# Optimization experiments

Hardware: AMD Instinct MI355X
Metric: run time of the kernel (lower is better)

The kernel has to match this reference:

```python
import jax, jax.numpy as jnp
import numpy as np

H, I, C, B, T = 128, 270, 3, 1024, 270


def setup_inputs() -> dict:
    key = jax.random.key(0)
    ks = jax.random.split(key, 6)
    inp = {
        "x": jax.random.normal(ks[0], (B, T, I), dtype=jnp.float32),
        "Wf": jax.random.normal(ks[1], (H, I + H), dtype=jnp.float32) * 0.01,
        "Wi": jax.random.normal(ks[2], (H, I + H), dtype=jnp.float32) * 0.01,
        "Wc": jax.random.normal(ks[3], (H, I + H), dtype=jnp.float32) * 0.01,
        "Wo": jax.random.normal(ks[4], (H, I + H), dtype=jnp.float32) * 0.01,
        "Wy": jax.random.normal(ks[5], (C, H), dtype=jnp.float32) * 0.01,
        "bf": jnp.zeros((H,), jnp.float32),
        "bi": jnp.zeros((H,), jnp.float32),
        "bc": jnp.zeros((H,), jnp.float32),
        "bo": jnp.zeros((H,), jnp.float32),
        "by": jnp.zeros((C,), jnp.float32),
    }
    return inp


def _lstm_forward(x, Wf, Wi, Wc, Wo, Wy, bf, bi, bc, bo, by):
    # combined = [h_prev, x_t], so W[:, :H] acts on h, W[:, H:] acts on x.
    Wh = jnp.stack([Wf[:, :H], Wi[:, :H], Wc[:, :H], Wo[:, :H]])      # [4,H,H]
    Wx = jnp.stack([Wf[:, H:], Wi[:, H:], Wc[:, H:], Wo[:, H:]])      # [4,H,I]
    b = jnp.stack([bf, bi, bc, bo])                                   # [4,H]
    # Precompute input projections for all timesteps: one big GEMM.
    xp = jnp.einsum('bti,ghi->tbgh', x, Wx)                           # [T,B,4,H]

    def step(carry, xpt):
        h, c = carry
        pre = xpt + jnp.einsum('bh,gkh->bgk', h, Wh) + b              # [B,4,H]
        f = jax.nn.sigmoid(pre[:, 0])
        i = jax.nn.sigmoid(pre[:, 1])
        g = jnp.tanh(pre[:, 2])
        o = jax.nn.sigmoid(pre[:, 3])
        c_new = f * c + i * g
        h_new = o * jnp.tanh(c_new)
        return (h_new, c_new), h_new

    h0 = jnp.zeros((x.shape[0], H), x.dtype)
    c0 = jnp.zeros((x.shape[0], H), x.dtype)
    _, hs = jax.lax.scan(step, (h0, c0), xp)                          # hs: [T,B,H]
    all_hiddens = jnp.transpose(hs, (1, 0, 2))                        # [B,T,H]
    logits = jnp.einsum('bth,ch->btc', all_hiddens, Wy) + by
    all_outputs = jax.nn.softmax(logits, axis=-1)                     # [B,T,C]
    return all_hiddens, all_outputs


def reference(x, Wf, Wi, Wc, Wo, Wy, bf, bi, bc, bo, by):
    return _lstm_forward(x, Wf, Wi, Wc, Wo, Wy, bf, bi, bc, bo, by)
```

## Files before the change

### kernel.cpp

```cpp
#include <hip/hip_runtime.h>
#include <stdint.h>


typedef __attribute__((ext_vector_type(8))) short short8;
typedef __attribute__((ext_vector_type(4))) float f32x4;
typedef __attribute__((ext_vector_type(2))) float f32x2;
typedef __attribute__((ext_vector_type(4))) unsigned int uint4v;
typedef __attribute__((ext_vector_type(2))) unsigned int u32x2;
typedef unsigned short ush;

__device__ __forceinline__ ush f2bf(float f) {
    unsigned u = __float_as_uint(f);
    return (ush)((u + 0x7FFFu + ((u >> 16) & 1u)) >> 16);
}
__device__ __forceinline__ float bf2f(ush s) { return __uint_as_float(((unsigned)s) << 16); }
__device__ __forceinline__ void lds_barrier() {
    asm volatile("s_waitcnt lgkmcnt(0)" ::: "memory");
    __builtin_amdgcn_s_barrier();
    __builtin_amdgcn_sched_barrier(0);
    asm volatile("" ::: "memory");
}

__global__ __launch_bounds__(256) void pack_w(
    const float* __restrict__ Wf, const float* __restrict__ Wi,
    const float* __restrict__ Wc, const float* __restrict__ Wo,
    const float* __restrict__ bf_, const float* __restrict__ bi_,
    const float* __restrict__ bc_, const float* __restrict__ bo_,
    ush* __restrict__ Wxp, ush* __restrict__ Whp, float* __restrict__ bpk)
{
    int idx = blockIdx.x * 256 + threadIdx.x;
    if (idx < 512 * 288) {
        int u = idx / 288, i = idx - u * 288;
        int g = u >> 7, j = u & 127;
        const float* Wg = (g == 0) ? Wf : (g == 1) ? Wi : (g == 2) ? Wc : Wo;
        float v = (i < 270) ? Wg[(size_t)j * 398 + 128 + i] : 0.f;
        Wxp[idx] = f2bf(v);
    }
    if (idx < 512 * 128) {
        int u = idx >> 7, k = idx & 127;
        int g = u >> 7, j = u & 127;
        const float* Wg = (g == 0) ? Wf : (g == 1) ? Wi : (g == 2) ? Wc : Wo;
        Whp[idx] = f2bf(Wg[(size_t)j * 398 + k]);
    }
    if (idx < 512) {
        int g = idx >> 7, j = idx & 127;
        const float* bg = (g == 0) ? bf_ : (g == 1) ? bi_ : (g == 2) ? bc_ : bo_;
        bpk[idx] = bg[j];
    }
}

__global__ __launch_bounds__(256, 2) void xp_gemm(
    const float* __restrict__ x, const ush* __restrict__ Wxp,
    const float* __restrict__ bpk, ush* __restrict__ xpc, int t0)
{
    __shared__ ush A_lds[64 * 296];
    const int tid = threadIdx.x;
    const int l = tid & 63, w = tid >> 6;
    const int l16 = l & 15, lq = l >> 4;
    const size_t row0 = (size_t)blockIdx.x * 64;

    const int srow = tid >> 2, sgrp = tid & 3;
    const int r = (int)row0 + srow;
    const int b = r & 1023, tt = (r >> 10) + t0;
    const float* xrow = x + ((size_t)b * 270 + tt) * 270;
    f32x2 stg[9][4];
    #pragma unroll
    for (int ks = 0; ks < 9; ++ks) {
        const int col = ks * 32 + sgrp * 8;
        const float* p = xrow + col;
        if (col + 8 <= 270) {
            stg[ks][0] = *(const f32x2*)p;       stg[ks][1] = *(const f32x2*)(p + 2);
            stg[ks][2] = *(const f32x2*)(p + 4); stg[ks][3] = *(const f32x2*)(p + 6);
        } else {
            float tv[8];
            #pragma unroll
            for (int j = 0; j < 8; ++j) tv[j] = (col + j < 270) ? p[j] : 0.f;
            stg[ks][0] = (f32x2){tv[0], tv[1]}; stg[ks][1] = (f32x2){tv[2], tv[3]};
            stg[ks][2] = (f32x2){tv[4], tv[5]}; stg[ks][3] = (f32x2){tv[6], tv[7]};
        }
    }

    const ush* bptr = Wxp + ((size_t)(w * 128 + l16)) * 288 + lq * 8;
    short8 bA[8], bB[8];
    #pragma unroll
    for (int nt = 0; nt < 8; ++nt) bA[nt] = *(const short8*)(bptr + nt * 4608);
    float bias_v[8];
    #pragma unroll
    for (int nt = 0; nt < 8; ++nt) bias_v[nt] = bpk[w * 128 + nt * 16 + l16];

    {
        ush* wrow = &A_lds[srow * 296 + sgrp * 8];
        #pragma unroll
        for (int ks = 0; ks < 9; ++ks) {
            uint4v o;
            #pragma unroll
            for (int p2 = 0; p2 < 4; ++p2) {
                unsigned v;
                asm("v_cvt_pk_bf16_f32 %0, %1, %2"
                    : "=v"(v) : "v"(stg[ks][p2].x), "v"(stg[ks][p2].y));
                o[p2] = v;
            }
            *(uint4v*)(wrow + ks * 32) = o;
        }
    }
    lds_barrier();

    f32x4 acc[4][8];
    #pragma unroll
    for (int mt = 0; mt < 4; ++mt)
        #pragma unroll
        for (int nt = 0; nt < 8; ++nt)
            acc[mt][nt] = (f32x4){bias_v[nt], bias_v[nt], bias_v[nt], bias_v[nt]};

    #pragma unroll
    for (int ks = 0; ks < 9; ++ks) {
        short8* cur = (ks & 1) ? bB : bA;
        short8* nxt = (ks & 1) ? bA : bB;
        if (ks + 1 < 9) {
            const ush* np = bptr + (ks + 1) * 32;
            #pragma unroll
            for (int nt = 0; nt < 8; ++nt) nxt[nt] = *(const short8*)(np + nt * 4608);
        }
        short8 afr[4];
        #pragma unroll
        for (int mt = 0; mt < 4; ++mt)
            afr[mt] = *(const short8*)(&A_lds[(mt * 16 + l16) * 296 + ks * 32 + lq * 8]);
        #pragma unroll
        for (int mt = 0; mt < 4; ++mt)
            #pragma unroll
            for (int nt = 0; nt < 8; ++nt)
                acc[mt][nt] = __builtin_amdgcn_mfma_f32_16x16x32_bf16(
                    afr[mt], cur[nt], acc[mt][nt], 0, 0, 0);
    }

    const int tloc = (int)(row0 >> 10);
    const int bg0 = ((int)row0 & 1023) >> 4;
    #pragma unroll
    for (int mt = 0; mt < 4; ++mt)
        #pragma unroll
        for (int nt = 0; nt < 8; ++nt) {
            int u = w * 128 + nt * 16 + l16;
            ush* dst = xpc + ((size_t)(tloc * 64 + bg0 + mt) * 512 + u) * 16 + lq * 4;
            #pragma unroll
            for (int q = 0; q < 4; ++q) dst[q] = f2bf(acc[mt][nt][q]);
        }
}

#define STEPB(T, PS)                                                            \
  {                                                                             \
    const int t_ = (T);                                                         \
    const bool lw_ = (((w >> 2) ^ (t_ & 1)) == 0) && (t_ > t0);                 \
    short8 afr[4];                                                              \
    _Pragma("unroll") for (int kf = 0; kf < 4; ++kf) {                          \
      int off_ = ((l16 * 128 + kf * 32 + lq * 8) * 2) ^ ((l16 & 7) << 4);       \
      afr[kf] = *(const short8*)(hbase + cur * 4096 + off_);                    \
    }                                                                           \
    float xg_[4][4];                                                            \
    _Pragma("unroll") for (int g = 0; g < 4; ++g) {                             \
      u32x2 pv_ = PS[g];                                                        \
      xg_[g][0] = __uint_as_float(pv_.x << 16);                                 \
      xg_[g][1] = __uint_as_float(pv_.x & 0xffff0000u);                         \
      xg_[g][2] = __uint_as_float(pv_.y << 16);                                 \
      xg_[g][3] = __uint_as_float(pv_.y & 0xffff0000u);                         \
    }                                                                           \
    if (t_ + 2 < t1) {                                                          \
      const ush* pn_ = xb + (size_t)(t_ + 2 - t0) * TSTEP;                      \
      _Pragma("unroll") for (int g = 0; g < 4; ++g)                             \
        PS[g] = *(const u32x2*)(pn_ + go[g]);                                   \
    }                                                                           \
    f32x4 a0_[4], a1_[4];                                                       \
    _Pragma("unroll") for (int g = 0; g < 4; ++g) {                             \
      a0_[g] = (f32x4){xg_[g][0], xg_[g][1], xg_[g][2], xg_[g][3]};             \
      a1_[g] = (f32x4){0.f, 0.f, 0.f, 0.f};                                     \
    }                                                                           \
    _Pragma("unroll") for (int g = 0; g < 4; ++g) {                             \
      a0_[g] = __builtin_amdgcn_mfma_f32_16x16x32_bf16(afr[0], whf[g][0], a0_[g], 0, 0, 0); \
      a1_[g] = __builtin_amdgcn_mfma_f32_16x16x32_bf16(afr[2], whf[g][2], a1_[g], 0, 0, 0); \
      a0_[g] = __builtin_amdgcn_mfma_f32_16x16x32_bf16(afr[1], whf[g][1], a0_[g], 0, 0, 0); \
      a1_[g] = __builtin_amdgcn_mfma_f32_16x16x32_bf16(afr[3], whf[g][3], a1_[g], 0, 0, 0); \
    }                                                                           \
    f32x4 ay0_ = (f32x4){0.f, 0.f, 0.f, 0.f};                                   \
    f32x4 ay1_ = (f32x4){0.f, 0.f, 0.f, 0.f};                                   \
    if (lw_) {                            \
      ay0_ = __builtin_amdgcn_mfma_f32_16x16x32_bf16(afr[0], wyf[0], ay0_, 0, 0, 0); \
      ay1_ = __builtin_amdgcn_mfma_f32_16x16x32_bf16(afr[2], wyf[2], ay1_, 0, 0, 0); \
      ay0_ = __builtin_amdgcn_mfma_f32_16x16x32_bf16(afr[1], wyf[1], ay0_, 0, 0, 0); \
      ay1_ = __builtin_amdgcn_mfma_f32_16x16x32_bf16(afr[3], wyf[3], ay1_, 0, 0, 0); \
    }                                                                           \
    float hv_[4];                                                               \
    _Pragma("unroll") for (int q = 0; q < 4; ++q) {                             \
      float pf_ = fminf(fmaxf(a0_[0][q] + a1_[0][q], -20.f), 20.f);             \
      float pi_ = fminf(fmaxf(a0_[1][q] + a1_[1][q], -20.f), 20.f);             \
      float pc_ = fminf(fmaxf(a0_[2][q] + a1_[2][q], -10.f), 10.f);             \
      float po_ = fminf(fmaxf(a0_[3][q] + a1_[3][q], -20.f), 20.f);             \
      float df_ = 1.f + __expf(-pf_);                                           \
      float di_ = 1.f + __expf(-pi_);                                           \
      float ec2_ = __expf(-2.f * pc_);                                          \
      float dc_ = 1.f + ec2_;                                                   \
      float do2_ = 1.f + __expf(-po_);                                          \
      float didc_ = di_ * dc_;                                                  \
      float num_ = c[q] * didc_ + (1.f - ec2_) * df_;                           \
      float cn_ = num_ * __builtin_amdgcn_rcpf(df_ * didc_);                    \
      c[q] = cn_;                                                               \
      float cnc_ = fminf(fmaxf(cn_, -10.f), 10.f);                              \
      float et2_ = __expf(-2.f * cnc_);                                         \
      hv_[q] = (1.f - et2_) * __builtin_amdgcn_rcpf(do2_ * (1.f + et2_));       \
    }                                                                           \
    _Pragma("unroll") for (int q = 0; q < 4; ++q) {                             \
      int rr_ = lq * 4 + q;                                                     \
      int off_ = ((rr_ * 128 + jcol) * 2) ^ ((rr_ & 7) << 4);                   \
      *(ush*)(hbase + (cur ^ 1) * 4096 + off_) = f2bf(hv_[q]);                  \
      out0[(size_t)(b0 + rr_) * (270 * 128) + (size_t)t_ * 128 + jcol] = hv_[q];\
    }                                                                           \
    lds_barrier();                                                              \
       \
    if (lw_) {                                                                  \
      f32x4 ay_ = ay0_ + ay1_;                                                  \
      int ww_ = w & 3;                                                          \
      float L_ = ((ww_ == 0) ? ay_[0] : (ww_ == 1) ? ay_[1] : (ww_ == 2) ? ay_[2] : ay_[3]) + byl; \
      if (l16 >= 3) L_ = -1e30f;                                                \
      float m_ = fmaxf(L_, __shfl_xor(L_, 1));                                  \
      m_ = fmaxf(m_, __shfl_xor(m_, 2));                                        \
      float e_ = (l16 < 3) ? __expf(L_ - m_) : 0.f;                             \
      float s_ = e_ + __shfl_xor(e_, 1);                                        \
      s_ = s_ + __shfl_xor(s_, 2);                                              \
      if (l16 < 3)                                                              \
        out1[((size_t)(b0 + lq * 4 + ww_) * 270 + (t_ - 1)) * 3 + l16] = e_ * __builtin_amdgcn_rcpf(s_); \
    }                                                                           \
    cur ^= 1;                                                                   \
  }

__global__ __launch_bounds__(512) void lstm_scan(
    const ush* __restrict__ xpc, const ush* __restrict__ Whp,
    float* __restrict__ c_state, float* __restrict__ out0, float* __restrict__ out1,
    const float* __restrict__ Wy, const float* __restrict__ by, int t0, int t1)
{
    __shared__ ush h_lds[2][16 * 128];
    const int tid = threadIdx.x;
    const int l = tid & 63, w = tid >> 6;
    const int l16 = l & 15, lq = l >> 4;
    const int b0 = blockIdx.x * 16;
    const int jcol = w * 16 + l16;
    char* hbase = (char*)&h_lds[0][0];

    short8 whf[4][4];
    #pragma unroll
    for (int g = 0; g < 4; ++g) {
        const ush* bw = Whp + ((size_t)(g * 128 + jcol)) * 128 + lq * 8;
        #pragma unroll
        for (int kf = 0; kf < 4; ++kf) whf[g][kf] = *(const short8*)(bw + kf * 32);
    }
    short8 wyf[4];
    #pragma unroll
    for (int kf = 0; kf < 4; ++kf) {
        short8 fr;
        #pragma unroll
        for (int j = 0; j < 8; ++j)
            fr[j] = (l16 < 3) ? (short)f2bf(Wy[l16 * 128 + kf * 32 + lq * 8 + j]) : (short)0;
        wyf[kf] = fr;
    }
    const float byl = (l16 < 3) ? by[l16] : 0.f;

    {
        ush* hp = &h_lds[0][0];
        for (int idx = tid; idx < 2 * 16 * 128; idx += 512) hp[idx] = 0;
    }
    __syncthreads();

    int cur = 0;
    float c[4] = {0.f, 0.f, 0.f, 0.f};
    if (t0 != 0) {
        #pragma unroll
        for (int q = 0; q < 4; ++q)
            c[q] = c_state[(size_t)(b0 + lq * 4 + q) * 128 + jcol];
        for (int idx = tid; idx < 2048; idx += 512) {
            int rr = idx >> 7, k = idx & 127;
            float hvv = out0[(size_t)(b0 + rr) * (270 * 128) + (size_t)(t0 - 1) * 128 + k];
            int off = ((rr * 128 + k) * 2) ^ ((rr & 7) << 4);
            *(ush*)(hbase + off) = f2bf(hvv);
        }
        __syncthreads();
    }

    const size_t TSTEP = (size_t)64 * 512 * 16;
    const ush* xb = xpc + (size_t)blockIdx.x * 8192;
    int go[4];
    #pragma unroll
    for (int g = 0; g < 4; ++g) go[g] = (g * 128 + jcol) * 16 + lq * 4;

    u32x2 Pa[4], Pb[4];
    #pragma unroll
    for (int g = 0; g < 4; ++g) Pa[g] = *(const u32x2*)(xb + go[g]);
    #pragma unroll
    for (int g = 0; g < 4; ++g) Pb[g] = *(const u32x2*)(xb + TSTEP + go[g]);

    for (int t = t0; t < t1; t += 2) {
        STEPB(t, Pa)
        STEPB(t + 1, Pb)
    }

    {
        short8 afr[4];
        #pragma unroll
        for (int kf = 0; kf < 4; ++kf) {
            int off = ((l16 * 128 + kf * 32 + lq * 8) * 2) ^ ((l16 & 7) << 4);
            afr[kf] = *(const short8*)(hbase + cur * 4096 + off);
        }
        if (w < 4) {
            f32x4 ay = (f32x4){0.f, 0.f, 0.f, 0.f};
            ay = __builtin_amdgcn_mfma_f32_16x16x32_bf16(afr[0], wyf[0], ay, 0, 0, 0);
            ay = __builtin_amdgcn_mfma_f32_16x16x32_bf16(afr[1], wyf[1], ay, 0, 0, 0);
            ay = __builtin_amdgcn_mfma_f32_16x16x32_bf16(afr[2], wyf[2], ay, 0, 0, 0);
            ay = __builtin_amdgcn_mfma_f32_16x16x32_bf16(afr[3], wyf[3], ay, 0, 0, 0);
            float L = ((w == 0) ? ay[0] : (w == 1) ? ay[1] : (w == 2) ? ay[2] : ay[3]) + byl;
            if (l16 >= 3) L = -1e30f;
            float m = fmaxf(L, __shfl_xor(L, 1));
            m = fmaxf(m, __shfl_xor(m, 2));
            float e = (l16 < 3) ? __expf(L - m) : 0.f;
            float s = e + __shfl_xor(e, 1);
            s = s + __shfl_xor(s, 2);
            if (l16 < 3)
                out1[((size_t)(b0 + lq * 4 + w) * 270 + (t1 - 1)) * 3 + l16] =
                    e * __builtin_amdgcn_rcpf(s);
        }
    }

    if (t1 != 270) {
        #pragma unroll
        for (int q = 0; q < 4; ++q)
            c_state[(size_t)(b0 + lq * 4 + q) * 128 + jcol] = c[q];
    }
}

extern "C" void kernel_launch(void* const* d_in, const int* in_sizes, int n_in,
                              void* d_out, int out_size, void* d_ws, size_t ws_size,
                              hipStream_t stream) {
    (void)in_sizes; (void)n_in; (void)out_size;
    const float* x   = (const float*)d_in[0];
    const float* Wf  = (const float*)d_in[1];
    const float* Wi  = (const float*)d_in[2];
    const float* Wc  = (const float*)d_in[3];
    const float* Wo  = (const float*)d_in[4];
    const float* Wy  = (const float*)d_in[5];
    const float* bfp = (const float*)d_in[6];
    const float* bip = (const float*)d_in[7];
    const float* bcp = (const float*)d_in[8];
    const float* bop = (const float*)d_in[9];
    const float* byp = (const float*)d_in[10];

    float* out0 = (float*)d_out;
    float* out1 = out0 + (size_t)1024 * 270 * 128;

    long tc = 6;
    {
        const long cand[6] = {270, 90, 54, 30, 18, 6};
        for (int i = 0; i < 6; ++i) {
            size_t need = (size_t)cand[i] * 1048576u + (2u << 20);
            if (need <= ws_size) { tc = cand[i]; break; }
        }
    }
    char* wsb = (char*)d_ws;
    ush* xpc = (ush*)wsb;
    char* fx = wsb + (size_t)tc * 1048576u;
    float* c_state = (float*)fx;
    ush* Wxp = (ush*)(fx + 524288);
    ush* Whp = (ush*)(fx + 524288 + 294912);
    float* bpk = (float*)(fx + 524288 + 294912 + 131072);

    pack_w<<<576, 256, 0, stream>>>(Wf, Wi, Wc, Wo, bfp, bip, bcp, bop, Wxp, Whp, bpk);

    for (int t0 = 0; t0 < 270; t0 += (int)tc) {
        int Tcur = (270 - t0) < (int)tc ? (270 - t0) : (int)tc;
        int rows = Tcur * 1024;
        xp_gemm<<<rows / 64, 256, 0, stream>>>(x, Wxp, bpk, xpc, t0);
        lstm_scan<<<64, 512, 0, stream>>>(xpc, Whp, c_state, out0, out1, Wy, byp,
                                          t0, t0 + Tcur);
    }
}
```

Before: 477.4 us.

## Split LSTM scan across 256 blocks of 4 batch rows, gate exchange via LDS

The recurrent scan now gives each block 4 batch rows instead of 16, so 256 blocks are launched instead of 64. The MFMA still computes a 16-row tile, but only the first 4 rows are valid. Gate pre-activations go through LDS so each thread handles one (row, unit) element, and the xp GEMM output layout changes to interleave the four gates per unit. The aim is to use more CUs on the serial time loop. The cost is an extra LDS barrier per step and three quarters of the MFMA work wasted on padding rows.

After: 578.7 us. 1.21x slower.

```diff
diff --git a/kernel.cpp b/kernel.cpp
--- a/kernel.cpp
+++ b/kernel.cpp
@@ -13,7 +13,6 @@
     unsigned u = __float_as_uint(f);
     return (ush)((u + 0x7FFFu + ((u >> 16) & 1u)) >> 16);
 }
-__device__ __forceinline__ float bf2f(ush s) { return __uint_as_float(((unsigned)s) << 16); }
 __device__ __forceinline__ void lds_barrier() {
     asm volatile("s_waitcnt lgkmcnt(0)" ::: "memory");
     __builtin_amdgcn_s_barrier();
@@ -133,44 +132,31 @@
                     afr[mt], cur[nt], acc[mt][nt], 0, 0, 0);
     }
 
-    const int tloc = (int)(row0 >> 10);
-    const int bg0 = ((int)row0 & 1023) >> 4;
     #pragma unroll
     for (int mt = 0; mt < 4; ++mt)
         #pragma unroll
         for (int nt = 0; nt < 8; ++nt) {
-            int u = w * 128 + nt * 16 + l16;
-            ush* dst = xpc + ((size_t)(tloc * 64 + bg0 + mt) * 512 + u) * 16 + lq * 4;
-            #pragma unroll
-            for (int q = 0; q < 4; ++q) dst[q] = f2bf(acc[mt][nt][q]);
+            int uu = nt * 16 + l16;
+            #pragma unroll
+            for (int q = 0; q < 4; ++q) {
+                size_t rg = row0 + mt * 16 + lq * 4 + q;
+                xpc[(rg * 128 + uu) * 4 + w] = f2bf(acc[mt][nt][q]);
+            }
         }
 }
 
 #define STEPB(T, PS)                                                            \
   {                                                                             \
     const int t_ = (T);                                                         \
-    const bool lw_ = (((w >> 2) ^ (t_ & 1)) == 0) && (t_ > t0);                 \
+    const bool lw_ = (t_ > t0) && (w == 4 * (t_ & 1));                          \
     short8 afr[4];                                                              \
     _Pragma("unroll") for (int kf = 0; kf < 4; ++kf) {                          \
       int off_ = ((l16 * 128 + kf * 32 + lq * 8) * 2) ^ ((l16 & 7) << 4);       \
       afr[kf] = *(const short8*)(hbase + cur * 4096 + off_);                    \
     }                                                                           \
-    float xg_[4][4];                                                            \
-    _Pragma("unroll") for (int g = 0; g < 4; ++g) {                             \
-      u32x2 pv_ = PS[g];                                                        \
-      xg_[g][0] = __uint_as_float(pv_.x << 16);                                 \
-      xg_[g][1] = __uint_as_float(pv_.x & 0xffff0000u);                         \
-      xg_[g][2] = __uint_as_float(pv_.y << 16);                                 \
-      xg_[g][3] = __uint_as_float(pv_.y & 0xffff0000u);                         \
-    }                                                                           \
-    if (t_ + 2 < t1) {                                                          \
-      const ush* pn_ = xb + (size_t)(t_ + 2 - t0) * TSTEP;                      \
-      _Pragma("unroll") for (int g = 0; g < 4; ++g)                             \
-        PS[g] = *(const u32x2*)(pn_ + go[g]);                                   \
-    }                                                                           \
     f32x4 a0_[4], a1_[4];                                                       \
     _Pragma("unroll") for (int g = 0; g < 4; ++g) {                             \
-      a0_[g] = (f32x4){xg_[g][0], xg_[g][1], xg_[g][2], xg_[g][3]};             \
+      a0_[g] = (f32x4){0.f, 0.f, 0.f, 0.f};                                     \
       a1_[g] = (f32x4){0.f, 0.f, 0.f, 0.f};                                     \
     }                                                                           \
     _Pragma("unroll") for (int g = 0; g < 4; ++g) {                             \
@@ -187,45 +173,59 @@
       ay0_ = __builtin_amdgcn_mfma_f32_16x16x32_bf16(afr[1], wyf[1], ay0_, 0, 0, 0); \
       ay1_ = __builtin_amdgcn_mfma_f32_16x16x32_bf16(afr[3], wyf[3], ay1_, 0, 0, 0); \
     }                                                                           \
-    float hv_[4];                                                               \
-    _Pragma("unroll") for (int q = 0; q < 4; ++q) {                             \
-      float pf_ = fminf(fmaxf(a0_[0][q] + a1_[0][q], -20.f), 20.f);             \
-      float pi_ = fminf(fmaxf(a0_[1][q] + a1_[1][q], -20.f), 20.f);             \
-      float pc_ = fminf(fmaxf(a0_[2][q] + a1_[2][q], -10.f), 10.f);             \
-      float po_ = fminf(fmaxf(a0_[3][q] + a1_[3][q], -20.f), 20.f);             \
+    if (lq == 0) {               \
+      _Pragma("unroll") for (int q = 0; q < 4; ++q) {                           \
+        f32x4 pv;                                                               \
+        pv.x = a0_[0][q] + a1_[0][q];                                           \
+        pv.y = a0_[1][q] + a1_[1][q];                                           \
+        pv.z = a0_[2][q] + a1_[2][q];                                           \
+        pv.w = a0_[3][q] + a1_[3][q];                                           \
+        *(f32x4*)(&pre_lds[q][w * 16 + l16][0]) = pv;                           \
+      }                                                                         \
+    }                                                                           \
+    lds_barrier();                                                              \
+    f32x4 pr_ = *(const f32x4*)(&pre_lds[row][unit][0]);                        \
+    u32x2 pv_ = PS;                                                             \
+    float xgf_ = __uint_as_float(pv_.x << 16);                                  \
+    float xgi_ = __uint_as_float(pv_.x & 0xffff0000u);                          \
+    float xgc_ = __uint_as_float(pv_.y << 16);                                  \
+    float xgo_ = __uint_as_float(pv_.y & 0xffff0000u);                          \
+    if (t_ + 2 < t1) PS = *(const u32x2*)(xq + (size_t)(t_ + 2 - t0) * TSTEP);  \
+    {                                                                           \
+      float pf_ = fminf(fmaxf(pr_.x + xgf_, -20.f), 20.f);                      \
+      float pi_ = fminf(fmaxf(pr_.y + xgi_, -20.f), 20.f);                      \
+      float pc_ = fminf(fmaxf(pr_.z + xgc_, -10.f), 10.f);                      \
+      float po_ = fminf(fmaxf(pr_.w + xgo_, -20.f), 20.f);                      \
       float df_ = 1.f + __expf(-pf_);                                           \
       float di_ = 1.f + __expf(-pi_);                                           \
       float ec2_ = __expf(-2.f * pc_);                                          \
       float dc_ = 1.f + ec2_;                                                   \
       float do2_ = 1.f + __expf(-po_);                                          \
       float didc_ = di_ * dc_;                                                  \
-      float num_ = c[q] * didc_ + (1.f - ec2_) * df_;                           \
+      float num_ = c1 * didc_ + (1.f - ec2_) * df_;                             \
       float cn_ = num_ * __builtin_amdgcn_rcpf(df_ * didc_);                    \
-      c[q] = cn_;                                                               \
+      c1 = cn_;                                                                 \
       float cnc_ = fminf(fmaxf(cn_, -10.f), 10.f);                              \
       float et2_ = __expf(-2.f * cnc_);                                         \
-      hv_[q] = (1.f - et2_) * __builtin_amdgcn_rcpf(do2_ * (1.f + et2_));       \
-    }                                                                           \
-    _Pragma("unroll") for (int q = 0; q < 4; ++q) {                             \
-      int rr_ = lq * 4 + q;                                                     \
-      int off_ = ((rr_ * 128 + jcol) * 2) ^ ((rr_ & 7) << 4);                   \
-      *(ush*)(hbase + (cur ^ 1) * 4096 + off_) = f2bf(hv_[q]);                  \
-      out0[(size_t)(b0 + rr_) * (270 * 128) + (size_t)t_ * 128 + jcol] = hv_[q];\
+      float hv_ = (1.f - et2_) * __builtin_amdgcn_rcpf(do2_ * (1.f + et2_));    \
+      int off_ = ((row * 128 + unit) * 2) ^ ((row & 7) << 4);                   \
+      *(ush*)(hbase + (cur ^ 1) * 4096 + off_) = f2bf(hv_);                     \
+      out0[(size_t)(b0 + row) * (270 * 128) + (size_t)t_ * 128 + unit] = hv_;   \
     }                                                                           \
     lds_barrier();                                                              \
-       \
-    if (lw_) {                                                                  \
+    if (lw_ && lq == 0) {           \
       f32x4 ay_ = ay0_ + ay1_;                                                  \
-      int ww_ = w & 3;                                                          \
-      float L_ = ((ww_ == 0) ? ay_[0] : (ww_ == 1) ? ay_[1] : (ww_ == 2) ? ay_[2] : ay_[3]) + byl; \
-      if (l16 >= 3) L_ = -1e30f;                                                \
-      float m_ = fmaxf(L_, __shfl_xor(L_, 1));                                  \
-      m_ = fmaxf(m_, __shfl_xor(m_, 2));                                        \
-      float e_ = (l16 < 3) ? __expf(L_ - m_) : 0.f;                             \
-      float s_ = e_ + __shfl_xor(e_, 1);                                        \
-      s_ = s_ + __shfl_xor(s_, 2);                                              \
-      if (l16 < 3)                                                              \
-        out1[((size_t)(b0 + lq * 4 + ww_) * 270 + (t_ - 1)) * 3 + l16] = e_ * __builtin_amdgcn_rcpf(s_); \
+      _Pragma("unroll") for (int q = 0; q < 4; ++q) {                           \
+        float L_ = ay_[q] + byl;                                                \
+        if (l16 >= 3) L_ = -1e30f;                                              \
+        float m_ = fmaxf(L_, __shfl_xor(L_, 1));                                \
+        m_ = fmaxf(m_, __shfl_xor(m_, 2));                                      \
+        float e_ = (l16 < 3) ? __expf(L_ - m_) : 0.f;                           \
+        float s_ = e_ + __shfl_xor(e_, 1);                                      \
+        s_ = s_ + __shfl_xor(s_, 2);                                            \
+        if (l16 < 3)                                                            \
+          out1[((size_t)(b0 + q) * 270 + (t_ - 1)) * 3 + l16] = e_ * __builtin_amdgcn_rcpf(s_); \
+      }                                                                         \
     }                                                                           \
     cur ^= 1;                                                                   \
   }
@@ -236,10 +236,13 @@
     const float* __restrict__ Wy, const float* __restrict__ by, int t0, int t1)
 {
     __shared__ ush h_lds[2][16 * 128];
+    __shared__ float pre_lds[4][128][4];
     const int tid = threadIdx.x;
     const int l = tid & 63, w = tid >> 6;
     const int l16 = l & 15, lq = l >> 4;
-    const int b0 = blockIdx.x * 16;
+    const int b0 = blockIdx.x * 4;
+    const int row = tid >> 7;
+    const int unit = tid & 127;
     const int jcol = w * 16 + l16;
     char* hbase = (char*)&h_lds[0][0];
 
@@ -268,68 +271,56 @@
     __syncthreads();
 
     int cur = 0;
-    float c[4] = {0.f, 0.f, 0.f, 0.f};
+    float c1 = 0.f;
     if (t0 != 0) {
-        #pragma unroll
-        for (int q = 0; q < 4; ++q)
-            c[q] = c_state[(size_t)(b0 + lq * 4 + q) * 128 + jcol];
-        for (int idx = tid; idx < 2048; idx += 512) {
-            int rr = idx >> 7, k = idx & 127;
-            float hvv = out0[(size_t)(b0 + rr) * (270 * 128) + (size_t)(t0 - 1) * 128 + k];
-            int off = ((rr * 128 + k) * 2) ^ ((rr & 7) << 4);
-            *(ush*)(hbase + off) = f2bf(hvv);
-        }
+        c1 = c_state[(size_t)(b0 + row) * 128 + unit];
+        float hvv = out0[(size_t)(b0 + row) * (270 * 128) + (size_t)(t0 - 1) * 128 + unit];
+        int off = ((row * 128 + unit) * 2) ^ ((row & 7) << 4);
+        *(ush*)(hbase + off) = f2bf(hvv);
         __syncthreads();
     }
 
-    const size_t TSTEP = (size_t)64 * 512 * 16;
-    const ush* xb = xpc + (size_t)blockIdx.x * 8192;
-    int go[4];
-    #pragma unroll
-    for (int g = 0; g < 4; ++g) go[g] = (g * 128 + jcol) * 16 + lq * 4;
-
-    u32x2 Pa[4], Pb[4];
-    #pragma unroll
-    for (int g = 0; g < 4; ++g) Pa[g] = *(const u32x2*)(xb + go[g]);
-    #pragma unroll
-    for (int g = 0; g < 4; ++g) Pb[g] = *(const u32x2*)(xb + TSTEP + go[g]);
+    const size_t TSTEP = (size_t)1024 * 128 * 4;
+    const ush* xq = xpc + ((size_t)(b0 + row) * 128 + unit) * 4;
+    u32x2 Pa = *(const u32x2*)(xq);
+    u32x2 Pb = *(const u32x2*)(xq + TSTEP);
 
     for (int t = t0; t < t1; t += 2) {
         STEPB(t, Pa)
         STEPB(t + 1, Pb)
     }
 
-    {
+    if (w == 0) {
         short8 afr[4];
         #pragma unroll
         for (int kf = 0; kf < 4; ++kf) {
             int off = ((l16 * 128 + kf * 32 + lq * 8) * 2) ^ ((l16 & 7) << 4);
             afr[kf] = *(const short8*)(hbase + cur * 4096 + off);
         }
-        if (w < 4) {
-            f32x4 ay = (f32x4){0.f, 0.f, 0.f, 0.f};
-            ay = __builtin_amdgcn_mfma_f32_16x16x32_bf16(afr[0], wyf[0], ay, 0, 0, 0);
-            ay = __builtin_amdgcn_mfma_f32_16x16x32_bf16(afr[1], wyf[1], ay, 0, 0, 0);
-            ay = __builtin_amdgcn_mfma_f32_16x16x32_bf16(afr[2], wyf[2], ay, 0, 0, 0);
-            ay = __builtin_amdgcn_mfma_f32_16x16x32_bf16(afr[3], wyf[3], ay, 0, 0, 0);
-            float L = ((w == 0) ? ay[0] : (w == 1) ? ay[1] : (w == 2) ? ay[2] : ay[3]) + byl;
-            if (l16 >= 3) L = -1e30f;
-            float m = fmaxf(L, __shfl_xor(L, 1));
-            m = fmaxf(m, __shfl_xor(m, 2));
-            float e = (l16 < 3) ? __expf(L - m) : 0.f;
-            float s = e + __shfl_xor(e, 1);
-            s = s + __shfl_xor(s, 2);
-            if (l16 < 3)
-                out1[((size_t)(b0 + lq * 4 + w) * 270 + (t1 - 1)) * 3 + l16] =
-                    e * __builtin_amdgcn_rcpf(s);
-        }
-    }
-
-    if (t1 != 270) {
-        #pragma unroll
-        for (int q = 0; q < 4; ++q)
-            c_state[(size_t)(b0 + lq * 4 + q) * 128 + jcol] = c[q];
-    }
+        f32x4 ay = (f32x4){0.f, 0.f, 0.f, 0.f};
+        ay = __builtin_amdgcn_mfma_f32_16x16x32_bf16(afr[0], wyf[0], ay, 0, 0, 0);
+        ay = __builtin_amdgcn_mfma_f32_16x16x32_bf16(afr[1], wyf[1], ay, 0, 0, 0);
+        ay = __builtin_amdgcn_mfma_f32_16x16x32_bf16(afr[2], wyf[2], ay, 0, 0, 0);
+        ay = __builtin_amdgcn_mfma_f32_16x16x32_bf16(afr[3], wyf[3], ay, 0, 0, 0);
+        if (lq == 0) {
+            #pragma unroll
+            for (int q = 0; q < 4; ++q) {
+                float L = ay[q] + byl;
+                if (l16 >= 3) L = -1e30f;
+                float m = fmaxf(L, __shfl_xor(L, 1));
+                m = fmaxf(m, __shfl_xor(m, 2));
+                float e = (l16 < 3) ? __expf(L - m) : 0.f;
+                float s = e + __shfl_xor(e, 1);
+                s = s + __shfl_xor(s, 2);
+                if (l16 < 3)
+                    out1[((size_t)(b0 + q) * 270 + (t1 - 1)) * 3 + l16] =
+                        e * __builtin_amdgcn_rcpf(s);
+            }
+        }
+    }
+
+    if (t1 != 270)
+        c_state[(size_t)(b0 + row) * 128 + unit] = c1;
 }
 
 extern "C" void kernel_launch(void* const* d_in, const int* in_sizes, int n_in,
@@ -373,7 +364,7 @@
         int Tcur = (270 - t0) < (int)tc ? (270 - t0) : (int)tc;
         int rows = Tcur * 1024;
         xp_gemm<<<rows / 64, 256, 0, stream>>>(x, Wxp, bpk, xpc, t0);
-        lstm_scan<<<64, 512, 0, stream>>>(xpc, Whp, c_state, out0, out1, Wy, byp,
-                                          t0, t0 + Tcur);
-    }
-}
+        lstm_scan<<<256, 512, 0, stream>>>(xpc, Whp, c_state, out0, out1, Wy, byp,
+                                           t0, t0 + Tcur);
+    }
+}
```
